# Performance work log

Hardware: AMD Instinct MI355X
Metric: run time of the kernel (lower is better)

The kernel has to match this reference:

```python
import jax, jax.numpy as jnp
import numpy as np

ALPHA = 0.2  # leaky_relu slope from GATLayer
NEG_INF = -9e15


def gat_layer(h, W, a, adj_mask, concat):
    """Faithful GATLayer.forward without the NxNx2F intermediate.

    h: [b, N, Fin], W: [Fin, Fout], a: [2*Fout], adj_mask: [b, N, N] bool.
    e[b,i,j] = leaky_relu(a[:F].Wh_i + a[F:].Wh_j)  (same math as torch concat version).
    """
    Wh = jnp.einsum('bnf,fo->bno', h, W)            # [b, N, Fout]
    Fo = W.shape[1]
    e1 = Wh @ a[:Fo]                                 # [b, N]  (source term)
    e2 = Wh @ a[Fo:]                                 # [b, N]  (target term)
    e = e1[:, :, None] + e2[:, None, :]              # [b, N, N]
    e = jax.nn.leaky_relu(e, negative_slope=ALPHA)
    e = jnp.where(adj_mask, e, NEG_INF)
    attn = jax.nn.softmax(e, axis=2)                 # softmax over neighbors j
    out = jnp.einsum('bij,bjo->bio', attn, Wh)       # [b, N, Fout]
    return jax.nn.elu(out) if concat else out


def setup_inputs() -> dict:
    key = jax.random.key(0)
    ks = jax.random.split(key, 6)
    b, N = 32, 512
    comp_dim, gat_dim, num_head = 80, 50, 3
    h = jax.random.normal(ks[0], (b, N, comp_dim), dtype=jnp.float32)
    adj = jax.random.randint(ks[1], (b, N, N), 0, 2, dtype=jnp.int32)
    s = 1.414 / np.sqrt(comp_dim)
    Ws = jax.random.uniform(ks[2], (num_head, comp_dim, gat_dim), jnp.float32, -s, s)
    attn_a = jax.random.uniform(ks[3], (num_head, 2 * gat_dim), jnp.float32, -0.2, 0.2)
    so = 1.414 / np.sqrt(gat_dim * num_head)
    W_out = jax.random.uniform(ks[4], (gat_dim * num_head, comp_dim), jnp.float32, -so, so)
    a_out = jax.random.uniform(ks[5], (2 * comp_dim,), jnp.float32, -0.15, 0.15)
    return {"h": h, "adj": adj, "Ws": Ws, "attn_a": attn_a, "W_out": W_out, "a_out": a_out}


def reference(h, adj, Ws, attn_a, W_out, a_out):
    adj_mask = adj > 0
    # num_head parallel GAT heads (concat=True), vmapped over the head axis
    heads = jax.vmap(lambda W, a: gat_layer(h, W, a, adj_mask, True))(Ws, attn_a)
    # [H, b, N, gat_dim] -> [b, N, H*gat_dim]
    Hn, b, N, Fo = heads.shape
    cat = jnp.transpose(heads, (1, 2, 0, 3)).reshape(b, N, Hn * Fo)
    # output GAT layer (concat=False -> no ELU)
    return gat_layer(cat, W_out, a_out, adj_mask, False)
```

## Files before the change

### kernel.cpp

```cpp
#include <hip/hip_runtime.h>
#include <stdint.h>

typedef unsigned long long u64;
typedef __attribute__((ext_vector_type(8))) short short8;
typedef __attribute__((ext_vector_type(4))) float f32x4;

#define B_ 32
#define N_ 512
#define FIN_ 80
#define FH_ 50
#define FO_ 80
#define CAT_ 150
#define KP_ 160
#define NP_ 96

__device__ inline unsigned short f2bf(float f) {
  unsigned u = __float_as_uint(f);
  u += 0x7fffu + ((u >> 16) & 1u);
  return (unsigned short)(u >> 16);
}

__device__ inline unsigned nib4(int4 v) {
  return (v.x != 0 ? 1u : 0u) | (v.y != 0 ? 2u : 0u) |
         (v.z != 0 ? 4u : 0u) | (v.w != 0 ? 8u : 0u);
}

__device__ inline short8 build_af(const float* e2s, float e1r, u64 word,
                                  int jb, int shift) {
  short8 af;
  unsigned b0 = (unsigned)(word >> shift) & 0xffu;
  float4 va = *(const float4*)&e2s[jb];
  float4 vb = *(const float4*)&e2s[jb + 4];
  float ev[8] = {va.x, va.y, va.z, va.w, vb.x, vb.y, vb.z, vb.w};
  #pragma unroll
  for (int e = 0; e < 8; ++e) {
    float sv = e1r + ev[e];
    sv = fmaxf(sv, 0.2f * sv);
    sv = fminf(sv, 60.f);
    float arg = ((b0 >> e) & 1u) ? sv : -1e30f;
    af[e] = (short)f2bf(__expf(arg));
  }
  return af;
}

__global__ __launch_bounds__(256) void k0_maskprep(const int* __restrict__ adj,
                                                   const float* __restrict__ Ws,
                                                   const float* __restrict__ attn_a,
                                                   const float* __restrict__ Wout,
                                                   const float* __restrict__ a_out,
                                                   u64* __restrict__ maskw,
                                                   unsigned short* __restrict__ WsT,
                                                   float* __restrict__ wa1g,
                                                   float* __restrict__ wa2g,
                                                   unsigned short* __restrict__ WoutT,
                                                   float* __restrict__ wv1,
                                                   float* __restrict__ wv2) {
  __shared__ unsigned short sm[256];
  const int t = threadIdx.x;
  const int bid = blockIdx.x;

  if (bid < 2048) {
    const int r = t >> 5, s = t & 31;
    const int row = bid * 8 + r;
    const int4* src = (const int4*)(adj + (size_t)row * N_ + s * 16);
    int4 v0 = src[0], v1 = src[1], v2 = src[2], v3 = src[3];
    unsigned m = nib4(v0) | (nib4(v1) << 4) | (nib4(v2) << 8) | (nib4(v3) << 12);
    sm[t] = (unsigned short)m;
    __syncthreads();
    if (t < 64) {
      const int rr = t >> 3, w = t & 7;
      const unsigned short* p = &sm[rr * 32 + w * 4];
      u64 mm = (u64)p[0] | ((u64)p[1] << 16) | ((u64)p[2] << 32) | ((u64)p[3] << 48);
      maskw[(size_t)(bid * 8 + rr) * 8 + w] = mm;
    }
    return;
  }

  const int pb = bid - 2048;
  if (pb < 15) {
    const int i = pb * 256 + t;
    const int base = i * 4;
    const int col = base / KP_, k0 = base % KP_;
    unsigned short pk[4];
    #pragma unroll
    for (int e = 0; e < 4; ++e) {
      const int k = k0 + e;
      pk[e] = (col < FO_ && k < CAT_) ? f2bf(Wout[(size_t)k * FO_ + col]) : 0;
    }
    uint2 o;
    o.x = (unsigned)pk[0] | ((unsigned)pk[1] << 16);
    o.y = (unsigned)pk[2] | ((unsigned)pk[3] << 16);
    ((uint2*)WoutT)[i] = o;
  } else if (pb < 24) {
    const int idx = (pb - 15) * 256 + t;
    const int hh = idx / 768, rem = idx - hh * 768;
    const int f = rem >> 6, lf = rem & 63;
    const int ks = f >> 2, nt = f & 3;
    const int kb = ks * 32 + (lf >> 4) * 8, n = nt * 16 + (lf & 15);
    const float* wsrc = Ws + (size_t)hh * FIN_ * FH_;
    short8 v8;
    #pragma unroll
    for (int e = 0; e < 8; ++e) {
      const int k = kb + e;
      v8[e] = (k < FIN_ && n < FH_) ? (short)f2bf(wsrc[k * FH_ + n]) : (short)0;
    }
    *(short8*)&WsT[(size_t)idx * 8] = v8;
  } else if (pb == 24) {
    if (t < 3 * FIN_) {
      const int hh = t / FIN_, k = t - hh * FIN_;
      const float* wr = Ws + ((size_t)hh * FIN_ + k) * FH_;
      const float* a1 = attn_a + hh * 2 * FH_;
      float s1 = 0.f, s2 = 0.f;
      #pragma unroll 10
      for (int c = 0; c < FH_; ++c) { s1 += wr[c] * a1[c]; s2 += wr[c] * a1[FH_ + c]; }
      wa1g[t] = s1; wa2g[t] = s2;
    }
  } else {
    if (t < CAT_) {
      const float4* wr = (const float4*)(Wout + (size_t)t * FO_);
      const float4* a1 = (const float4*)a_out;
      const float4* a2 = (const float4*)(a_out + FO_);
      float p1 = 0.f, p2 = 0.f;
      #pragma unroll
      for (int i = 0; i < 20; ++i) {
        float4 v = wr[i], x1 = a1[i], x2 = a2[i];
        p1 += v.x * x1.x + v.y * x1.y + v.z * x1.z + v.w * x1.w;
        p2 += v.x * x2.x + v.y * x2.y + v.z * x2.z + v.w * x2.w;
      }
      wv1[t] = p1; wv2[t] = p2;
    }
  }
}

__global__ __launch_bounds__(256) void k1_mfma(const float* __restrict__ h,
                                               const unsigned short* __restrict__ WsT,
                                               const float* __restrict__ wa1g,
                                               const float* __restrict__ wa2g,
                                               unsigned short* __restrict__ whT,
                                               float* __restrict__ e1h,
                                               float* __restrict__ e2h) {
  __shared__ __align__(16) unsigned short un[64 * 104];
  const int t = threadIdx.x;
  int x = blockIdx.x;
  const int rt = x & 7; x >>= 3;
  const int bb = x & 31; x >>= 5;
  const int hh = x;
  const int n0 = rt * 64;
  const float* hblk = h + ((size_t)bb * N_ + n0) * FIN_;

  for (int idx = t; idx < 64 * 13; idx += 256) {
    const int row = idx / 13, k0 = (idx - row * 13) * 8;
    short8 v8;
    if (k0 < FIN_) {
      float4 a = *(const float4*)(hblk + row * FIN_ + k0);
      float4 b = *(const float4*)(hblk + row * FIN_ + k0 + 4);
      v8[0] = (short)f2bf(a.x); v8[1] = (short)f2bf(a.y);
      v8[2] = (short)f2bf(a.z); v8[3] = (short)f2bf(a.w);
      v8[4] = (short)f2bf(b.x); v8[5] = (short)f2bf(b.y);
      v8[6] = (short)f2bf(b.z); v8[7] = (short)f2bf(b.w);
    } else {
      #pragma unroll
      for (int e = 0; e < 8; ++e) v8[e] = 0;
    }
    *(short8*)&un[row * 104 + k0] = v8;
  }
  __syncthreads();

  {
    const int r = t >> 2, cq = t & 3;
    const float* hr = hblk + r * FIN_ + cq * 20;
    const float4* w1 = (const float4*)(wa1g + hh * FIN_ + cq * 20);
    const float4* w2 = (const float4*)(wa2g + hh * FIN_ + cq * 20);
    float s1 = 0.f, s2 = 0.f;
    #pragma unroll
    for (int i = 0; i < 5; ++i) {
      float4 hv = *(const float4*)(hr + i * 4);
      float4 a = w1[i], b = w2[i];
      s1 += hv.x * a.x + hv.y * a.y + hv.z * a.z + hv.w * a.w;
      s2 += hv.x * b.x + hv.y * b.y + hv.z * b.z + hv.w * b.w;
    }
    s1 += __shfl_xor(s1, 1); s1 += __shfl_xor(s1, 2);
    s2 += __shfl_xor(s2, 1); s2 += __shfl_xor(s2, 2);
    if (cq == 0) {
      size_t o = ((size_t)hh * B_ + bb) * N_ + n0 + r;
      e1h[o] = s1; e2h[o] = s2;
    }
  }

  const int l = t & 63, wv = t >> 6, q = l >> 4, rl = l & 15;
  f32x4 acc[4];
  {
    short8 af[3];
    #pragma unroll
    for (int ks = 0; ks < 3; ++ks)
      af[ks] = *(const short8*)&un[(wv * 16 + rl) * 104 + ks * 32 + q * 8];
    #pragma unroll
    for (int nt = 0; nt < 4; ++nt) acc[nt] = (f32x4){0.f, 0.f, 0.f, 0.f};
    const unsigned short* wsb = WsT + (size_t)hh * 12 * 512;
    #pragma unroll
    for (int ks = 0; ks < 3; ++ks)
      #pragma unroll
      for (int nt = 0; nt < 4; ++nt)
        acc[nt] = __builtin_amdgcn_mfma_f32_16x16x32_bf16(
            af[ks], *(const short8*)&wsb[((ks * 4 + nt) * 64 + l) * 8], acc[nt], 0, 0, 0);
  }
  __syncthreads();
  unsigned short* tbT = un;
  #pragma unroll
  for (int nt = 0; nt < 4; ++nt)
    #pragma unroll
    for (int r2 = 0; r2 < 4; ++r2)
      tbT[(nt * 16 + rl) * 72 + wv * 16 + q * 4 + r2] = f2bf(acc[nt][r2]);
  __syncthreads();
  {
    const int col = t & 63, half = t >> 6;
    uint4 o0 = *(const uint4*)&tbT[col * 72 + half * 16];
    uint4 o1 = *(const uint4*)&tbT[col * 72 + half * 16 + 8];
    if (col == 63) {
      o0.x = o0.y = o0.z = o0.w = 0x3f803f80u;
      o1 = o0;
    }
    unsigned short* dst = whT + (((size_t)hh * B_ + bb) * 64 + col) * 512 + n0 + half * 16;
    *(uint4*)dst = o0;
    *(uint4*)(dst + 8) = o1;
  }
}

__global__ __launch_bounds__(256) void k3s(const unsigned short* __restrict__ whT,
                                           const float* __restrict__ e1,
                                           const float* __restrict__ e2,
                                           const u64* __restrict__ maskw,
                                           const float* __restrict__ wv1,
                                           const float* __restrict__ wv2,
                                           unsigned short* __restrict__ catbf,
                                           float* __restrict__ e1p,
                                           float* __restrict__ e2p) {
  __shared__ __align__(16) float e2s[N_];
  __shared__ __align__(16) float red[4][64][17];
  int x = (int)((blockIdx.x & 7) * 384 + (blockIdx.x >> 3));
  const int hh = x >> 10;
  const int bb = (x >> 5) & 31;
  const int rg = x & 31;
  const int n0 = rg * 16;
  const int t = threadIdx.x;
  const int l = t & 63, wid = t >> 6;
  const int q = l >> 4, rl = l & 15;

  const float* e2pp = e2 + ((size_t)hh * B_ + bb) * N_;
  for (int i = t; i < N_ / 4; i += 256) ((float4*)e2s)[i] = ((const float4*)e2pp)[i];
  __syncthreads();

  const int row = n0 + rl;
  const float e1r = e1[((size_t)hh * B_ + bb) * N_ + row];
  const u64* mr = maskw + ((size_t)bb * N_ + row) * 8;

  f32x4 acc[4];
  #pragma unroll
  for (int c = 0; c < 4; ++c) acc[c] = (f32x4){0.f, 0.f, 0.f, 0.f};
  const unsigned short* wb = whT + ((size_t)hh * B_ + bb) * 64 * 512;

  #pragma unroll
  for (int tts = 0; tts < 2; ++tts) {
    const int tt = wid * 2 + tts;
    short8 bf[4][2];
    #pragma unroll
    for (int c = 0; c < 4; ++c) {
      const unsigned short* bp = wb + (size_t)(c * 16 + rl) * 512 + tt * 64 + q * 8;
      bf[c][0] = *(const short8*)bp;
      bf[c][1] = *(const short8*)(bp + 32);
    }
    u64 word = mr[tt];
    short8 af0 = build_af(e2s, e1r, word, tt * 64 + q * 8, q * 8);
    short8 af1 = build_af(e2s, e1r, word, tt * 64 + 32 + q * 8, 32 + q * 8);
    #pragma unroll
    for (int c = 0; c < 4; ++c) {
      acc[c] = __builtin_amdgcn_mfma_f32_16x16x32_bf16(af0, bf[c][0], acc[c], 0, 0, 0);
      acc[c] = __builtin_amdgcn_mfma_f32_16x16x32_bf16(af1, bf[c][1], acc[c], 0, 0, 0);
    }
  }

  #pragma unroll
  for (int c = 0; c < 4; ++c)
    #pragma unroll
    for (int r = 0; r < 4; ++r) red[wid][l][c * 4 + r] = acc[c][r];
  __syncthreads();

  if (wid == 0) {
    #pragma unroll
    for (int c = 0; c < 4; ++c)
      #pragma unroll
      for (int r = 0; r < 4; ++r)
        acc[c][r] = red[0][l][c * 4 + r] + red[1][l][c * 4 + r] +
                    red[2][l][c * 4 + r] + red[3][l][c * 4 + r];
    float w1c[4], w2c[4];
    #pragma unroll
    for (int c = 0; c < 4; ++c) {
      const int col = c * 16 + rl;
      w1c[c] = (col < FH_) ? wv1[hh * FH_ + col] : 0.f;
      w2c[c] = (col < FH_) ? wv2[hh * FH_ + col] : 0.f;
    }
    #pragma unroll
    for (int r = 0; r < 4; ++r) {
      float srow = __shfl(acc[3][r], (q << 4) | 15);
      float invr = srow > 0.f ? 1.f / srow : 0.f;
      const size_t grow = (size_t)bb * N_ + n0 + q * 4 + r;
      float p1 = 0.f, p2 = 0.f;
      #pragma unroll
      for (int c = 0; c < 4; ++c) {
        const int col = c * 16 + rl;
        if (col < FH_) {
          float v = acc[c][r] * invr;
          v = v > 0.f ? v : __expf(v) - 1.f;
          catbf[grow * KP_ + hh * FH_ + col] = f2bf(v);
          p1 += v * w1c[c];
          p2 += v * w2c[c];
        }
      }
      p1 += __shfl_xor(p1, 1); p1 += __shfl_xor(p1, 2);
      p1 += __shfl_xor(p1, 4); p1 += __shfl_xor(p1, 8);
      p2 += __shfl_xor(p2, 1); p2 += __shfl_xor(p2, 2);
      p2 += __shfl_xor(p2, 4); p2 += __shfl_xor(p2, 8);
      if (rl == 0) {
        e1p[(size_t)hh * (B_ * N_) + grow] = p1;
        e2p[(size_t)hh * (B_ * N_) + grow] = p2;
      }
    }
  }
  if (hh == 2 && t < 16) {
    const size_t grow = (size_t)bb * N_ + n0 + t;
    unsigned* zp = (unsigned*)&catbf[grow * KP_ + CAT_];
    #pragma unroll
    for (int i = 0; i < 5; ++i) zp[i] = 0u;
  }
}

__global__ __launch_bounds__(256) void k4_gemm2(const unsigned short* __restrict__ catbf,
                                                const unsigned short* __restrict__ WoutT,
                                                unsigned short* __restrict__ wh2T) {
  const int t = threadIdx.x, l = t & 63, wid = t >> 6;
  const int q = l >> 4, rl = l & 15;
  const int blk = blockIdx.x;
  const int jbase = blk * 64 + wid * 16;
  f32x4 acc[5];
  #pragma unroll
  for (int nt = 0; nt < 5; ++nt) acc[nt] = (f32x4){0.f, 0.f, 0.f, 0.f};
  const unsigned short* ap = catbf + (size_t)(jbase + rl) * KP_ + q * 8;
  #pragma unroll
  for (int kk = 0; kk < 5; ++kk) {
    short8 a = *(const short8*)(ap + kk * 32);
    #pragma unroll
    for (int nt = 0; nt < 5; ++nt) {
      short8 b = *(const short8*)&WoutT[(size_t)(nt * 16 + rl) * KP_ + kk * 32 + q * 8];
      acc[nt] = __builtin_amdgcn_mfma_f32_16x16x32_bf16(a, b, acc[nt], 0, 0, 0);
    }
  }
  const int bb = blk >> 3, jt = blk & 7;
  const int j0 = jt * 64 + wid * 16 + q * 4;
  #pragma unroll
  for (int nt = 0; nt < 5; ++nt) {
    const int col = nt * 16 + rl;
    unsigned short pk[4];
    #pragma unroll
    for (int r = 0; r < 4; ++r) pk[r] = f2bf(acc[nt][r]);
    uint2 o;
    o.x = (unsigned)pk[0] | ((unsigned)pk[1] << 16);
    o.y = (unsigned)pk[2] | ((unsigned)pk[3] << 16);
    *(uint2*)&wh2T[((size_t)bb * NP_ + col) * 512 + j0] = o;
  }
  {
    const int col = 80 + (t >> 4), jq = (t & 15) * 4;
    unsigned fill = (col == 95) ? 0x3f803f80u : 0u;
    uint2 o; o.x = fill; o.y = fill;
    *(uint2*)&wh2T[((size_t)bb * NP_ + col) * 512 + jt * 64 + jq] = o;
  }
}

__global__ __launch_bounds__(256) void k5_attn2(const unsigned short* __restrict__ wh2T,
                                                const float* __restrict__ e1p,
                                                const float* __restrict__ e2p,
                                                const u64* __restrict__ maskw,
                                                float* __restrict__ out) {
  __shared__ __align__(16) float e2s[N_];
  __shared__ __align__(16) float red[4][64][25];
  int x = (int)((blockIdx.x & 7) * 128 + (blockIdx.x >> 3));
  const int rg = x & 31;
  const int bb = x >> 5;
  const int n0 = rg * 16;
  const int t = threadIdx.x;
  const int l = t & 63, wid = t >> 6;
  const int q = l >> 4, rl = l & 15;

  for (int i = t; i < N_ / 4; i += 256) {
    float4 v0 = ((const float4*)(e2p))[(size_t)bb * 128 + i];
    float4 v1 = ((const float4*)(e2p + B_ * N_))[(size_t)bb * 128 + i];
    float4 v2 = ((const float4*)(e2p + 2 * B_ * N_))[(size_t)bb * 128 + i];
    float4 s;
    s.x = v0.x + v1.x + v2.x; s.y = v0.y + v1.y + v2.y;
    s.z = v0.z + v1.z + v2.z; s.w = v0.w + v1.w + v2.w;
    ((float4*)e2s)[i] = s;
  }
  __syncthreads();

  const int row = n0 + rl;
  const size_t gr = (size_t)bb * N_ + row;
  const float e1r = e1p[gr] + e1p[B_ * N_ + gr] + e1p[2 * B_ * N_ + gr];
  const u64* mr = maskw + gr * 8;

  f32x4 acc[6];
  #pragma unroll
  for (int c = 0; c < 6; ++c) acc[c] = (f32x4){0.f, 0.f, 0.f, 0.f};
  const unsigned short* wb = wh2T + (size_t)bb * NP_ * 512;

  #pragma unroll
  for (int tts = 0; tts < 2; ++tts) {
    const int tt = wid * 2 + tts;
    short8 bf[6][2];
    #pragma unroll
    for (int c = 0; c < 6; ++c) {
      const unsigned short* bp = wb + (size_t)(c * 16 + rl) * 512 + tt * 64 + q * 8;
      bf[c][0] = *(const short8*)bp;
      bf[c][1] = *(const short8*)(bp + 32);
    }
    u64 word = mr[tt];
    short8 af0 = build_af(e2s, e1r, word, tt * 64 + q * 8, q * 8);
    short8 af1 = build_af(e2s, e1r, word, tt * 64 + 32 + q * 8, 32 + q * 8);
    #pragma unroll
    for (int c = 0; c < 6; ++c) {
      acc[c] = __builtin_amdgcn_mfma_f32_16x16x32_bf16(af0, bf[c][0], acc[c], 0, 0, 0);
      acc[c] = __builtin_amdgcn_mfma_f32_16x16x32_bf16(af1, bf[c][1], acc[c], 0, 0, 0);
    }
  }

  #pragma unroll
  for (int c = 0; c < 6; ++c)
    #pragma unroll
    for (int r = 0; r < 4; ++r) red[wid][l][c * 4 + r] = acc[c][r];
  __syncthreads();

  if (wid == 0) {
    #pragma unroll
    for (int c = 0; c < 6; ++c)
      #pragma unroll
      for (int r = 0; r < 4; ++r)
        acc[c][r] = red[0][l][c * 4 + r] + red[1][l][c * 4 + r] +
                    red[2][l][c * 4 + r] + red[3][l][c * 4 + r];
    const size_t orow0 = (size_t)bb * N_ + n0;
    #pragma unroll
    for (int r = 0; r < 4; ++r) {
      float srow = __shfl(acc[5][r], (q << 4) | 15);
      float invr = srow > 0.f ? 1.f / srow : 0.f;
      const size_t ob = (orow0 + q * 4 + r) * FO_;
      #pragma unroll
      for (int c = 0; c < 5; ++c) out[ob + c * 16 + rl] = acc[c][r] * invr;
    }
  }
}

extern "C" void kernel_launch(void* const* d_in, const int* in_sizes, int n_in,
                              void* d_out, int out_size, void* d_ws, size_t ws_size,
                              hipStream_t stream) {
  const float* h    = (const float*)d_in[0];
  const int*   adj  = (const int*)d_in[1];
  const float* Ws   = (const float*)d_in[2];
  const float* aa   = (const float*)d_in[3];
  const float* Wout = (const float*)d_in[4];
  const float* aout = (const float*)d_in[5];

  char* ws = (char*)d_ws;
  unsigned short* whT   = (unsigned short*)(ws + 0);
  float* e1h            = (float*)(ws + 6291456);
  float* e2h            = (float*)(ws + 6488064);
  u64*   mk             = (u64*)  (ws + 6684672);
  unsigned short* catbf = (unsigned short*)(ws + 7733248);
  unsigned short* WoutT = (unsigned short*)(ws + 12976128);
  float* wv1            = (float*)(ws + 13008896);
  float* wv2            = (float*)(ws + 13009920);
  float* e1p            = (float*)(ws + 13010944);
  float* e2p            = (float*)(ws + 13207552);
  unsigned short* wh2T  = (unsigned short*)(ws + 13404160);
  unsigned short* WsT   = (unsigned short*)(ws + 16549888);
  float* wa1g           = (float*)(ws + 16586752);
  float* wa2g           = (float*)(ws + 16587776);

  hipLaunchKernelGGL(k0_maskprep, dim3(2074), dim3(256), 0, stream,
                     adj, Ws, aa, Wout, aout, mk, WsT, wa1g, wa2g, WoutT, wv1, wv2);
  hipLaunchKernelGGL(k1_mfma, dim3(768), dim3(256), 0, stream,
                     h, WsT, wa1g, wa2g, whT, e1h, e2h);
  hipLaunchKernelGGL(k3s, dim3(3072), dim3(256), 0, stream,
                     whT, e1h, e2h, mk, wv1, wv2, catbf, e1p, e2p);
  hipLaunchKernelGGL(k4_gemm2, dim3(256), dim3(256), 0, stream, catbf, WoutT, wh2T);
  hipLaunchKernelGGL(k5_attn2, dim3(1024), dim3(256), 0, stream,
                     wh2T, e1p, e2p, mk, (float*)d_out);
}
```

Before: 72.13 us.

## Fuse prep kernels and reassociate output layer to attend over concat features

Merges the mask/weight-prep kernel with the first-layer projection kernel. Each projection block now converts its head's W slice into LDS and derives e1/e2 from the MFMA accumulators instead of precomputed W·a vectors. The separate output GEMM kernel is removed: the final attention multiplies the attention weights against the transposed 160-wide concat features, with a ones-column as denominator, and then applies W_out per row tile via a second MFMA. This drops two launches and the wh2T intermediate, but widens the attention accumulation from 96 to 160 columns and makes the W_out projection redundant per block.

Result: slower. 75.76 us (+5.0%).

```diff
diff --git a/kernel.cpp b/kernel.cpp
--- a/kernel.cpp
+++ b/kernel.cpp
@@ -43,18 +43,21 @@
   return af;
 }
 
-__global__ __launch_bounds__(256) void k0_maskprep(const int* __restrict__ adj,
-                                                   const float* __restrict__ Ws,
-                                                   const float* __restrict__ attn_a,
-                                                   const float* __restrict__ Wout,
-                                                   const float* __restrict__ a_out,
-                                                   u64* __restrict__ maskw,
-                                                   unsigned short* __restrict__ WsT,
-                                                   float* __restrict__ wa1g,
-                                                   float* __restrict__ wa2g,
-                                                   unsigned short* __restrict__ WoutT,
-                                                   float* __restrict__ wv1,
-                                                   float* __restrict__ wv2) {
+__global__ __launch_bounds__(256) void kA(const float* __restrict__ h,
+                                          const int* __restrict__ adj,
+                                          const float* __restrict__ Ws,
+                                          const float* __restrict__ attn_a,
+                                          const float* __restrict__ Wout,
+                                          const float* __restrict__ a_out,
+                                          unsigned short* __restrict__ whT,
+                                          float* __restrict__ e1h,
+                                          float* __restrict__ e2h,
+                                          u64* __restrict__ maskw,
+                                          unsigned short* __restrict__ WoutT,
+                                          float* __restrict__ wv1,
+                                          float* __restrict__ wv2) {
+  __shared__ __align__(16) unsigned short un[64 * 104];
+  __shared__ __align__(16) unsigned short bstage[12 * 512];
   __shared__ unsigned short sm[256];
   const int t = threadIdx.x;
   const int bid = blockIdx.x;
@@ -75,10 +78,8 @@
     }
     return;
   }
-
-  const int pb = bid - 2048;
-  if (pb < 15) {
-    const int i = pb * 256 + t;
+  if (bid < 2063) {
+    const int i = (bid - 2048) * 256 + t;
     const int base = i * 4;
     const int col = base / KP_, k0 = base % KP_;
     unsigned short pk[4];
@@ -91,31 +92,9 @@
     o.x = (unsigned)pk[0] | ((unsigned)pk[1] << 16);
     o.y = (unsigned)pk[2] | ((unsigned)pk[3] << 16);
     ((uint2*)WoutT)[i] = o;
-  } else if (pb < 24) {
-    const int idx = (pb - 15) * 256 + t;
-    const int hh = idx / 768, rem = idx - hh * 768;
-    const int f = rem >> 6, lf = rem & 63;
-    const int ks = f >> 2, nt = f & 3;
-    const int kb = ks * 32 + (lf >> 4) * 8, n = nt * 16 + (lf & 15);
-    const float* wsrc = Ws + (size_t)hh * FIN_ * FH_;
-    short8 v8;
-    #pragma unroll
-    for (int e = 0; e < 8; ++e) {
-      const int k = kb + e;
-      v8[e] = (k < FIN_ && n < FH_) ? (short)f2bf(wsrc[k * FH_ + n]) : (short)0;
-    }
-    *(short8*)&WsT[(size_t)idx * 8] = v8;
-  } else if (pb == 24) {
-    if (t < 3 * FIN_) {
-      const int hh = t / FIN_, k = t - hh * FIN_;
-      const float* wr = Ws + ((size_t)hh * FIN_ + k) * FH_;
-      const float* a1 = attn_a + hh * 2 * FH_;
-      float s1 = 0.f, s2 = 0.f;
-      #pragma unroll 10
-      for (int c = 0; c < FH_; ++c) { s1 += wr[c] * a1[c]; s2 += wr[c] * a1[FH_ + c]; }
-      wa1g[t] = s1; wa2g[t] = s2;
-    }
-  } else {
+    return;
+  }
+  if (bid == 2063) {
     if (t < CAT_) {
       const float4* wr = (const float4*)(Wout + (size_t)t * FO_);
       const float4* a1 = (const float4*)a_out;
@@ -129,24 +108,16 @@
       }
       wv1[t] = p1; wv2[t] = p2;
     }
-  }
-}
-
-__global__ __launch_bounds__(256) void k1_mfma(const float* __restrict__ h,
-                                               const unsigned short* __restrict__ WsT,
-                                               const float* __restrict__ wa1g,
-                                               const float* __restrict__ wa2g,
-                                               unsigned short* __restrict__ whT,
-                                               float* __restrict__ e1h,
-                                               float* __restrict__ e2h) {
-  __shared__ __align__(16) unsigned short un[64 * 104];
-  const int t = threadIdx.x;
-  int x = blockIdx.x;
+    return;
+  }
+
+  int x = bid - 2064;
   const int rt = x & 7; x >>= 3;
   const int bb = x & 31; x >>= 5;
   const int hh = x;
   const int n0 = rt * 64;
   const float* hblk = h + ((size_t)bb * N_ + n0) * FIN_;
+  const float* wsrc = Ws + (size_t)hh * FIN_ * FH_;
 
   for (int idx = t; idx < 64 * 13; idx += 256) {
     const int row = idx / 13, k0 = (idx - row * 13) * 8;
@@ -164,28 +135,19 @@
     }
     *(short8*)&un[row * 104 + k0] = v8;
   }
-  __syncthreads();
-
-  {
-    const int r = t >> 2, cq = t & 3;
-    const float* hr = hblk + r * FIN_ + cq * 20;
-    const float4* w1 = (const float4*)(wa1g + hh * FIN_ + cq * 20);
-    const float4* w2 = (const float4*)(wa2g + hh * FIN_ + cq * 20);
-    float s1 = 0.f, s2 = 0.f;
-    #pragma unroll
-    for (int i = 0; i < 5; ++i) {
-      float4 hv = *(const float4*)(hr + i * 4);
-      float4 a = w1[i], b = w2[i];
-      s1 += hv.x * a.x + hv.y * a.y + hv.z * a.z + hv.w * a.w;
-      s2 += hv.x * b.x + hv.y * b.y + hv.z * b.z + hv.w * b.w;
-    }
-    s1 += __shfl_xor(s1, 1); s1 += __shfl_xor(s1, 2);
-    s2 += __shfl_xor(s2, 1); s2 += __shfl_xor(s2, 2);
-    if (cq == 0) {
-      size_t o = ((size_t)hh * B_ + bb) * N_ + n0 + r;
-      e1h[o] = s1; e2h[o] = s2;
-    }
-  }
+  for (int idx = t; idx < 768; idx += 256) {
+    const int f = idx >> 6, lf = idx & 63;
+    const int ks = f >> 2, nt = f & 3;
+    const int kb = ks * 32 + (lf >> 4) * 8, n = nt * 16 + (lf & 15);
+    short8 v8;
+    #pragma unroll
+    for (int e = 0; e < 8; ++e) {
+      const int k = kb + e;
+      v8[e] = (k < FIN_ && n < FH_) ? (short)f2bf(wsrc[k * FH_ + n]) : (short)0;
+    }
+    *(short8*)&bstage[idx * 8] = v8;
+  }
+  __syncthreads();
 
   const int l = t & 63, wv = t >> 6, q = l >> 4, rl = l & 15;
   f32x4 acc[4];
@@ -196,13 +158,36 @@
       af[ks] = *(const short8*)&un[(wv * 16 + rl) * 104 + ks * 32 + q * 8];
     #pragma unroll
     for (int nt = 0; nt < 4; ++nt) acc[nt] = (f32x4){0.f, 0.f, 0.f, 0.f};
-    const unsigned short* wsb = WsT + (size_t)hh * 12 * 512;
     #pragma unroll
     for (int ks = 0; ks < 3; ++ks)
       #pragma unroll
       for (int nt = 0; nt < 4; ++nt)
         acc[nt] = __builtin_amdgcn_mfma_f32_16x16x32_bf16(
-            af[ks], *(const short8*)&wsb[((ks * 4 + nt) * 64 + l) * 8], acc[nt], 0, 0, 0);
+            af[ks], *(const short8*)&bstage[((ks * 4 + nt) * 64 + l) * 8], acc[nt], 0, 0, 0);
+  }
+  {
+    float a1v[4], a2v[4];
+    #pragma unroll
+    for (int c = 0; c < 4; ++c) {
+      const int col = c * 16 + rl;
+      a1v[c] = (col < FH_) ? attn_a[hh * 2 * FH_ + col] : 0.f;
+      a2v[c] = (col < FH_) ? attn_a[hh * 2 * FH_ + FH_ + col] : 0.f;
+    }
+    #pragma unroll
+    for (int r = 0; r < 4; ++r) {
+      float p1 = acc[0][r] * a1v[0] + acc[1][r] * a1v[1] +
+                 acc[2][r] * a1v[2] + acc[3][r] * a1v[3];
+      float p2 = acc[0][r] * a2v[0] + acc[1][r] * a2v[1] +
+                 acc[2][r] * a2v[2] + acc[3][r] * a2v[3];
+      p1 += __shfl_xor(p1, 1); p1 += __shfl_xor(p1, 2);
+      p1 += __shfl_xor(p1, 4); p1 += __shfl_xor(p1, 8);
+      p2 += __shfl_xor(p2, 1); p2 += __shfl_xor(p2, 2);
+      p2 += __shfl_xor(p2, 4); p2 += __shfl_xor(p2, 8);
+      if (rl == 0) {
+        size_t o = ((size_t)hh * B_ + bb) * N_ + n0 + wv * 16 + q * 4 + r;
+        e1h[o] = p1; e2h[o] = p2;
+      }
+    }
   }
   __syncthreads();
   unsigned short* tbT = un;
@@ -232,7 +217,7 @@
                                            const u64* __restrict__ maskw,
                                            const float* __restrict__ wv1,
                                            const float* __restrict__ wv2,
-                                           unsigned short* __restrict__ catbf,
+                                           unsigned short* __restrict__ catT,
                                            float* __restrict__ e1p,
                                            float* __restrict__ e2p) {
   __shared__ __align__(16) float e2s[N_];
@@ -303,7 +288,8 @@
     for (int r = 0; r < 4; ++r) {
       float srow = __shfl(acc[3][r], (q << 4) | 15);
       float invr = srow > 0.f ? 1.f / srow : 0.f;
-      const size_t grow = (size_t)bb * N_ + n0 + q * 4 + r;
+      const int jrow = n0 + q * 4 + r;
+      const size_t grow = (size_t)bb * N_ + jrow;
       float p1 = 0.f, p2 = 0.f;
       #pragma unroll
       for (int c = 0; c < 4; ++c) {
@@ -311,7 +297,7 @@
         if (col < FH_) {
           float v = acc[c][r] * invr;
           v = v > 0.f ? v : __expf(v) - 1.f;
-          catbf[grow * KP_ + hh * FH_ + col] = f2bf(v);
+          catT[((size_t)bb * KP_ + hh * FH_ + col) * 512 + jrow] = f2bf(v);
           p1 += v * w1c[c];
           p2 += v * w2c[c];
         }
@@ -327,61 +313,23 @@
     }
   }
   if (hh == 2 && t < 16) {
-    const size_t grow = (size_t)bb * N_ + n0 + t;
-    unsigned* zp = (unsigned*)&catbf[grow * KP_ + CAT_];
-    #pragma unroll
-    for (int i = 0; i < 5; ++i) zp[i] = 0u;
-  }
-}
-
-__global__ __launch_bounds__(256) void k4_gemm2(const unsigned short* __restrict__ catbf,
-                                                const unsigned short* __restrict__ WoutT,
-                                                unsigned short* __restrict__ wh2T) {
-  const int t = threadIdx.x, l = t & 63, wid = t >> 6;
-  const int q = l >> 4, rl = l & 15;
-  const int blk = blockIdx.x;
-  const int jbase = blk * 64 + wid * 16;
-  f32x4 acc[5];
-  #pragma unroll
-  for (int nt = 0; nt < 5; ++nt) acc[nt] = (f32x4){0.f, 0.f, 0.f, 0.f};
-  const unsigned short* ap = catbf + (size_t)(jbase + rl) * KP_ + q * 8;
-  #pragma unroll
-  for (int kk = 0; kk < 5; ++kk) {
-    short8 a = *(const short8*)(ap + kk * 32);
-    #pragma unroll
-    for (int nt = 0; nt < 5; ++nt) {
-      short8 b = *(const short8*)&WoutT[(size_t)(nt * 16 + rl) * KP_ + kk * 32 + q * 8];
-      acc[nt] = __builtin_amdgcn_mfma_f32_16x16x32_bf16(a, b, acc[nt], 0, 0, 0);
-    }
-  }
-  const int bb = blk >> 3, jt = blk & 7;
-  const int j0 = jt * 64 + wid * 16 + q * 4;
-  #pragma unroll
-  for (int nt = 0; nt < 5; ++nt) {
-    const int col = nt * 16 + rl;
-    unsigned short pk[4];
-    #pragma unroll
-    for (int r = 0; r < 4; ++r) pk[r] = f2bf(acc[nt][r]);
-    uint2 o;
-    o.x = (unsigned)pk[0] | ((unsigned)pk[1] << 16);
-    o.y = (unsigned)pk[2] | ((unsigned)pk[3] << 16);
-    *(uint2*)&wh2T[((size_t)bb * NP_ + col) * 512 + j0] = o;
-  }
-  {
-    const int col = 80 + (t >> 4), jq = (t & 15) * 4;
-    unsigned fill = (col == 95) ? 0x3f803f80u : 0u;
-    uint2 o; o.x = fill; o.y = fill;
-    *(uint2*)&wh2T[((size_t)bb * NP_ + col) * 512 + jt * 64 + jq] = o;
-  }
-}
-
-__global__ __launch_bounds__(256) void k5_attn2(const unsigned short* __restrict__ wh2T,
-                                                const float* __restrict__ e1p,
-                                                const float* __restrict__ e2p,
-                                                const u64* __restrict__ maskw,
-                                                float* __restrict__ out) {
+    const int j = n0 + t;
+    #pragma unroll
+    for (int kc = CAT_; kc < KP_; ++kc)
+      catT[((size_t)bb * KP_ + kc) * 512 + j] = (kc == KP_ - 1) ? (unsigned short)0x3f80 : 0;
+  }
+}
+
+__global__ __launch_bounds__(256) void kC(const unsigned short* __restrict__ catT,
+                                          const unsigned short* __restrict__ WoutT,
+                                          const float* __restrict__ e1p,
+                                          const float* __restrict__ e2p,
+                                          const u64* __restrict__ maskw,
+                                          float* __restrict__ out) {
   __shared__ __align__(16) float e2s[N_];
-  __shared__ __align__(16) float red[4][64][25];
+  __shared__ __align__(16) float red[3][64][41];
+  __shared__ __align__(16) unsigned short pA[16 * 168];
+  __shared__ float denomLDS[16];
   int x = (int)((blockIdx.x & 7) * 128 + (blockIdx.x >> 3));
   const int rg = x & 31;
   const int bb = x >> 5;
@@ -406,52 +354,78 @@
   const float e1r = e1p[gr] + e1p[B_ * N_ + gr] + e1p[2 * B_ * N_ + gr];
   const u64* mr = maskw + gr * 8;
 
-  f32x4 acc[6];
-  #pragma unroll
-  for (int c = 0; c < 6; ++c) acc[c] = (f32x4){0.f, 0.f, 0.f, 0.f};
-  const unsigned short* wb = wh2T + (size_t)bb * NP_ * 512;
+  f32x4 acc[10];
+  #pragma unroll
+  for (int c = 0; c < 10; ++c) acc[c] = (f32x4){0.f, 0.f, 0.f, 0.f};
+  const unsigned short* cb = catT + (size_t)bb * KP_ * 512;
 
   #pragma unroll
   for (int tts = 0; tts < 2; ++tts) {
     const int tt = wid * 2 + tts;
-    short8 bf[6][2];
-    #pragma unroll
-    for (int c = 0; c < 6; ++c) {
-      const unsigned short* bp = wb + (size_t)(c * 16 + rl) * 512 + tt * 64 + q * 8;
-      bf[c][0] = *(const short8*)bp;
-      bf[c][1] = *(const short8*)(bp + 32);
-    }
     u64 word = mr[tt];
     short8 af0 = build_af(e2s, e1r, word, tt * 64 + q * 8, q * 8);
     short8 af1 = build_af(e2s, e1r, word, tt * 64 + 32 + q * 8, 32 + q * 8);
     #pragma unroll
-    for (int c = 0; c < 6; ++c) {
-      acc[c] = __builtin_amdgcn_mfma_f32_16x16x32_bf16(af0, bf[c][0], acc[c], 0, 0, 0);
-      acc[c] = __builtin_amdgcn_mfma_f32_16x16x32_bf16(af1, bf[c][1], acc[c], 0, 0, 0);
-    }
-  }
-
-  #pragma unroll
-  for (int c = 0; c < 6; ++c)
-    #pragma unroll
-    for (int r = 0; r < 4; ++r) red[wid][l][c * 4 + r] = acc[c][r];
+    for (int c = 0; c < 10; ++c) {
+      const unsigned short* bp = cb + (size_t)(c * 16 + rl) * 512 + tt * 64 + q * 8;
+      short8 b0 = *(const short8*)bp;
+      short8 b1 = *(const short8*)(bp + 32);
+      acc[c] = __builtin_amdgcn_mfma_f32_16x16x32_bf16(af0, b0, acc[c], 0, 0, 0);
+      acc[c] = __builtin_amdgcn_mfma_f32_16x16x32_bf16(af1, b1, acc[c], 0, 0, 0);
+    }
+  }
+
+  if (wid > 0) {
+    #pragma unroll
+    for (int c = 0; c < 10; ++c)
+      #pragma unroll
+      for (int r = 0; r < 4; ++r) red[wid - 1][l][c * 4 + r] = acc[c][r];
+  }
   __syncthreads();
 
   if (wid == 0) {
     #pragma unroll
-    for (int c = 0; c < 6; ++c)
+    for (int c = 0; c < 10; ++c)
+      #pragma unroll
+      for (int r = 0; r < 4; ++r) {
+        const int idx = c * 4 + r;
+        acc[c][r] += red[0][l][idx] + red[1][l][idx] + red[2][l][idx];
+      }
+    #pragma unroll
+    for (int c = 0; c < 10; ++c)
       #pragma unroll
       for (int r = 0; r < 4; ++r)
-        acc[c][r] = red[0][l][c * 4 + r] + red[1][l][c * 4 + r] +
-                    red[2][l][c * 4 + r] + red[3][l][c * 4 + r];
-    const size_t orow0 = (size_t)bb * N_ + n0;
+        pA[(q * 4 + r) * 168 + c * 16 + rl] = f2bf(acc[c][r]);
+    if (rl == 15) {
+      #pragma unroll
+      for (int r = 0; r < 4; ++r) denomLDS[q * 4 + r] = acc[9][r];
+    }
+  }
+  __syncthreads();
+
+  if (wid == 0) {
+    short8 af2[5];
+    #pragma unroll
+    for (int ks = 0; ks < 5; ++ks)
+      af2[ks] = *(const short8*)&pA[rl * 168 + ks * 32 + q * 8];
+    f32x4 acc2[5];
+    #pragma unroll
+    for (int nt = 0; nt < 5; ++nt) acc2[nt] = (f32x4){0.f, 0.f, 0.f, 0.f};
+    #pragma unroll
+    for (int ks = 0; ks < 5; ++ks)
+      #pragma unroll
+      for (int nt = 0; nt < 5; ++nt)
+        acc2[nt] = __builtin_amdgcn_mfma_f32_16x16x32_bf16(
+            af2[ks],
+            *(const short8*)&WoutT[(size_t)(nt * 16 + rl) * KP_ + ks * 32 + q * 8],
+            acc2[nt], 0, 0, 0);
     #pragma unroll
     for (int r = 0; r < 4; ++r) {
-      float srow = __shfl(acc[5][r], (q << 4) | 15);
-      float invr = srow > 0.f ? 1.f / srow : 0.f;
-      const size_t ob = (orow0 + q * 4 + r) * FO_;
-      #pragma unroll
-      for (int c = 0; c < 5; ++c) out[ob + c * 16 + rl] = acc[c][r] * invr;
+      const float dv = denomLDS[q * 4 + r];
+      const float invr = dv > 0.f ? 1.f / dv : 0.f;
+      const size_t ob = ((size_t)bb * N_ + n0 + q * 4 + r) * FO_;
+      #pragma unroll
+      for (int nt = 0; nt < 5; ++nt) out[ob + nt * 16 + rl] = acc2[nt][r] * invr;
     }
   }
 }
@@ -471,24 +445,17 @@
   float* e1h            = (float*)(ws + 6291456);
   float* e2h            = (float*)(ws + 6488064);
   u64*   mk             = (u64*)  (ws + 6684672);
-  unsigned short* catbf = (unsigned short*)(ws + 7733248);
+  unsigned short* catT  = (unsigned short*)(ws + 7733248);
   unsigned short* WoutT = (unsigned short*)(ws + 12976128);
   float* wv1            = (float*)(ws + 13008896);
   float* wv2            = (float*)(ws + 13009920);
   float* e1p            = (float*)(ws + 13010944);
   float* e2p            = (float*)(ws + 13207552);
-  unsigned short* wh2T  = (unsigned short*)(ws + 13404160);
-  unsigned short* WsT   = (unsigned short*)(ws + 16549888);
-  float* wa1g           = (float*)(ws + 16586752);
-  float* wa2g           = (float*)(ws + 16587776);
-
-  hipLaunchKernelGGL(k0_maskprep, dim3(2074), dim3(256), 0, stream,
-                     adj, Ws, aa, Wout, aout, mk, WsT, wa1g, wa2g, WoutT, wv1, wv2);
-  hipLaunchKernelGGL(k1_mfma, dim3(768), dim3(256), 0, stream,
-                     h, WsT, wa1g, wa2g, whT, e1h, e2h);
+
+  hipLaunchKernelGGL(kA, dim3(2832), dim3(256), 0, stream,
+                     h, adj, Ws, aa, Wout, aout, whT, e1h, e2h, mk, WoutT, wv1, wv2);
   hipLaunchKernelGGL(k3s, dim3(3072), dim3(256), 0, stream,
-                     whT, e1h, e2h, mk, wv1, wv2, catbf, e1p, e2p);
-  hipLaunchKernelGGL(k4_gemm2, dim3(256), dim3(256), 0, stream, catbf, WoutT, wh2T);
-  hipLaunchKernelGGL(k5_attn2, dim3(1024), dim3(256), 0, stream,
-                     wh2T, e1p, e2p, mk, (float*)d_out);
-}
+                     whT, e1h, e2h, mk, wv1, wv2, catT, e1p, e2p);
+  hipLaunchKernelGGL(kC, dim3(1024), dim3(256), 0, stream,
+                     catT, WoutT, e1p, e2p, mk, (float*)d_out);
+}
```

## Fuse mask prep and head projection GEMM into one kernel launch

Applied to the files above, without the earlier changes.

Merges the mask/weight-prep kernel and the first-layer MFMA projection kernel into a single launch. Each GEMM block now converts its head's Ws slice to bf16 directly into shared memory instead of reading a pre-packed global copy. The e1/e2 attention scores are now computed from the MFMA accumulators via cross-lane shuffles, replacing the separate fp32 dot product with precomputed W·a vectors. This removes one launch and a dependency boundary, but every GEMM block now redoes the Ws conversion, uses more shared memory, and e1/e2 are computed from fp32 accumulators of bf16-rounded inputs rather than in full fp32.

New measurement: 73.83 us. 1.02x slower.

```diff
diff --git a/kernel.cpp b/kernel.cpp
--- a/kernel.cpp
+++ b/kernel.cpp
@@ -43,23 +43,26 @@
   return af;
 }
 
-__global__ __launch_bounds__(256) void k0_maskprep(const int* __restrict__ adj,
-                                                   const float* __restrict__ Ws,
-                                                   const float* __restrict__ attn_a,
-                                                   const float* __restrict__ Wout,
-                                                   const float* __restrict__ a_out,
-                                                   u64* __restrict__ maskw,
-                                                   unsigned short* __restrict__ WsT,
-                                                   float* __restrict__ wa1g,
-                                                   float* __restrict__ wa2g,
-                                                   unsigned short* __restrict__ WoutT,
-                                                   float* __restrict__ wv1,
-                                                   float* __restrict__ wv2) {
-  __shared__ unsigned short sm[256];
+__global__ __launch_bounds__(256) void kA(const float* __restrict__ h,
+                                          const int* __restrict__ adj,
+                                          const float* __restrict__ Ws,
+                                          const float* __restrict__ attn_a,
+                                          const float* __restrict__ Wout,
+                                          const float* __restrict__ a_out,
+                                          unsigned short* __restrict__ whT,
+                                          float* __restrict__ e1h,
+                                          float* __restrict__ e2h,
+                                          u64* __restrict__ maskw,
+                                          unsigned short* __restrict__ WoutT,
+                                          float* __restrict__ wv1,
+                                          float* __restrict__ wv2) {
+  __shared__ __align__(16) unsigned short un[64 * 104];
+  __shared__ __align__(16) unsigned short bstage[12 * 512];
   const int t = threadIdx.x;
   const int bid = blockIdx.x;
 
   if (bid < 2048) {
+    unsigned short* sm = un;
     const int r = t >> 5, s = t & 31;
     const int row = bid * 8 + r;
     const int4* src = (const int4*)(adj + (size_t)row * N_ + s * 16);
@@ -75,10 +78,8 @@
     }
     return;
   }
-
-  const int pb = bid - 2048;
-  if (pb < 15) {
-    const int i = pb * 256 + t;
+  if (bid < 2063) {
+    const int i = (bid - 2048) * 256 + t;
     const int base = i * 4;
     const int col = base / KP_, k0 = base % KP_;
     unsigned short pk[4];
@@ -91,31 +92,9 @@
     o.x = (unsigned)pk[0] | ((unsigned)pk[1] << 16);
     o.y = (unsigned)pk[2] | ((unsigned)pk[3] << 16);
     ((uint2*)WoutT)[i] = o;
-  } else if (pb < 24) {
-    const int idx = (pb - 15) * 256 + t;
-    const int hh = idx / 768, rem = idx - hh * 768;
-    const int f = rem >> 6, lf = rem & 63;
-    const int ks = f >> 2, nt = f & 3;
-    const int kb = ks * 32 + (lf >> 4) * 8, n = nt * 16 + (lf & 15);
-    const float* wsrc = Ws + (size_t)hh * FIN_ * FH_;
-    short8 v8;
-    #pragma unroll
-    for (int e = 0; e < 8; ++e) {
-      const int k = kb + e;
-      v8[e] = (k < FIN_ && n < FH_) ? (short)f2bf(wsrc[k * FH_ + n]) : (short)0;
-    }
-    *(short8*)&WsT[(size_t)idx * 8] = v8;
-  } else if (pb == 24) {
-    if (t < 3 * FIN_) {
-      const int hh = t / FIN_, k = t - hh * FIN_;
-      const float* wr = Ws + ((size_t)hh * FIN_ + k) * FH_;
-      const float* a1 = attn_a + hh * 2 * FH_;
-      float s1 = 0.f, s2 = 0.f;
-      #pragma unroll 10
-      for (int c = 0; c < FH_; ++c) { s1 += wr[c] * a1[c]; s2 += wr[c] * a1[FH_ + c]; }
-      wa1g[t] = s1; wa2g[t] = s2;
-    }
-  } else {
+    return;
+  }
+  if (bid == 2063) {
     if (t < CAT_) {
       const float4* wr = (const float4*)(Wout + (size_t)t * FO_);
       const float4* a1 = (const float4*)a_out;
@@ -129,24 +108,16 @@
       }
       wv1[t] = p1; wv2[t] = p2;
     }
-  }
-}
-
-__global__ __launch_bounds__(256) void k1_mfma(const float* __restrict__ h,
-                                               const unsigned short* __restrict__ WsT,
-                                               const float* __restrict__ wa1g,
-                                               const float* __restrict__ wa2g,
-                                               unsigned short* __restrict__ whT,
-                                               float* __restrict__ e1h,
-                                               float* __restrict__ e2h) {
-  __shared__ __align__(16) unsigned short un[64 * 104];
-  const int t = threadIdx.x;
-  int x = blockIdx.x;
+    return;
+  }
+
+  int x = bid - 2064;
   const int rt = x & 7; x >>= 3;
   const int bb = x & 31; x >>= 5;
   const int hh = x;
   const int n0 = rt * 64;
   const float* hblk = h + ((size_t)bb * N_ + n0) * FIN_;
+  const float* wsrc = Ws + (size_t)hh * FIN_ * FH_;
 
   for (int idx = t; idx < 64 * 13; idx += 256) {
     const int row = idx / 13, k0 = (idx - row * 13) * 8;
@@ -164,28 +135,19 @@
     }
     *(short8*)&un[row * 104 + k0] = v8;
   }
-  __syncthreads();
-
-  {
-    const int r = t >> 2, cq = t & 3;
-    const float* hr = hblk + r * FIN_ + cq * 20;
-    const float4* w1 = (const float4*)(wa1g + hh * FIN_ + cq * 20);
-    const float4* w2 = (const float4*)(wa2g + hh * FIN_ + cq * 20);
-    float s1 = 0.f, s2 = 0.f;
-    #pragma unroll
-    for (int i = 0; i < 5; ++i) {
-      float4 hv = *(const float4*)(hr + i * 4);
-      float4 a = w1[i], b = w2[i];
-      s1 += hv.x * a.x + hv.y * a.y + hv.z * a.z + hv.w * a.w;
-      s2 += hv.x * b.x + hv.y * b.y + hv.z * b.z + hv.w * b.w;
-    }
-    s1 += __shfl_xor(s1, 1); s1 += __shfl_xor(s1, 2);
-    s2 += __shfl_xor(s2, 1); s2 += __shfl_xor(s2, 2);
-    if (cq == 0) {
-      size_t o = ((size_t)hh * B_ + bb) * N_ + n0 + r;
-      e1h[o] = s1; e2h[o] = s2;
-    }
-  }
+  for (int idx = t; idx < 768; idx += 256) {
+    const int f = idx >> 6, lf = idx & 63;
+    const int ks = f >> 2, nt = f & 3;
+    const int kb = ks * 32 + (lf >> 4) * 8, n = nt * 16 + (lf & 15);
+    short8 v8;
+    #pragma unroll
+    for (int e = 0; e < 8; ++e) {
+      const int k = kb + e;
+      v8[e] = (k < FIN_ && n < FH_) ? (short)f2bf(wsrc[k * FH_ + n]) : (short)0;
+    }
+    *(short8*)&bstage[idx * 8] = v8;
+  }
+  __syncthreads();
 
   const int l = t & 63, wv = t >> 6, q = l >> 4, rl = l & 15;
   f32x4 acc[4];
@@ -196,13 +158,36 @@
       af[ks] = *(const short8*)&un[(wv * 16 + rl) * 104 + ks * 32 + q * 8];
     #pragma unroll
     for (int nt = 0; nt < 4; ++nt) acc[nt] = (f32x4){0.f, 0.f, 0.f, 0.f};
-    const unsigned short* wsb = WsT + (size_t)hh * 12 * 512;
     #pragma unroll
     for (int ks = 0; ks < 3; ++ks)
       #pragma unroll
       for (int nt = 0; nt < 4; ++nt)
         acc[nt] = __builtin_amdgcn_mfma_f32_16x16x32_bf16(
-            af[ks], *(const short8*)&wsb[((ks * 4 + nt) * 64 + l) * 8], acc[nt], 0, 0, 0);
+            af[ks], *(const short8*)&bstage[((ks * 4 + nt) * 64 + l) * 8], acc[nt], 0, 0, 0);
+  }
+  {
+    float a1v[4], a2v[4];
+    #pragma unroll
+    for (int c = 0; c < 4; ++c) {
+      const int col = c * 16 + rl;
+      a1v[c] = (col < FH_) ? attn_a[hh * 2 * FH_ + col] : 0.f;
+      a2v[c] = (col < FH_) ? attn_a[hh * 2 * FH_ + FH_ + col] : 0.f;
+    }
+    #pragma unroll
+    for (int r = 0; r < 4; ++r) {
+      float p1 = acc[0][r] * a1v[0] + acc[1][r] * a1v[1] +
+                 acc[2][r] * a1v[2] + acc[3][r] * a1v[3];
+      float p2 = acc[0][r] * a2v[0] + acc[1][r] * a2v[1] +
+                 acc[2][r] * a2v[2] + acc[3][r] * a2v[3];
+      p1 += __shfl_xor(p1, 1); p1 += __shfl_xor(p1, 2);
+      p1 += __shfl_xor(p1, 4); p1 += __shfl_xor(p1, 8);
+      p2 += __shfl_xor(p2, 1); p2 += __shfl_xor(p2, 2);
+      p2 += __shfl_xor(p2, 4); p2 += __shfl_xor(p2, 8);
+      if (rl == 0) {
+        size_t o = ((size_t)hh * B_ + bb) * N_ + n0 + wv * 16 + q * 4 + r;
+        e1h[o] = p1; e2h[o] = p2;
+      }
+    }
   }
   __syncthreads();
   unsigned short* tbT = un;
@@ -478,14 +463,9 @@
   float* e1p            = (float*)(ws + 13010944);
   float* e2p            = (float*)(ws + 13207552);
   unsigned short* wh2T  = (unsigned short*)(ws + 13404160);
-  unsigned short* WsT   = (unsigned short*)(ws + 16549888);
-  float* wa1g           = (float*)(ws + 16586752);
-  float* wa2g           = (float*)(ws + 16587776);
-
-  hipLaunchKernelGGL(k0_maskprep, dim3(2074), dim3(256), 0, stream,
-                     adj, Ws, aa, Wout, aout, mk, WsT, wa1g, wa2g, WoutT, wv1, wv2);
-  hipLaunchKernelGGL(k1_mfma, dim3(768), dim3(256), 0, stream,
-                     h, WsT, wa1g, wa2g, whT, e1h, e2h);
+
+  hipLaunchKernelGGL(kA, dim3(2832), dim3(256), 0, stream,
+                     h, adj, Ws, aa, Wout, aout, whT, e1h, e2h, mk, WoutT, wv1, wv2);
   hipLaunchKernelGGL(k3s, dim3(3072), dim3(256), 0, stream,
                      whT, e1h, e2h, mk, wv1, wv2, catbf, e1p, e2p);
   hipLaunchKernelGGL(k4_gemm2, dim3(256), dim3(256), 0, stream, catbf, WoutT, wh2T);
```
